# Kernel optimization log

Hardware: AMD Instinct MI355X
Metric: run time of the kernel (lower is better)

The kernel has to match this reference:

```python
import jax, jax.numpy as jnp
import numpy as np

D_MODEL = 768
NUM_HEADS = 12
DEPTH = D_MODEL // NUM_HEADS
LN_EPS = 1e-5


def setup_inputs() -> dict:
    key = jax.random.key(0)
    ks = jax.random.split(key, 5)
    B, S = 2, 2048
    scale = 1.0 / np.sqrt(D_MODEL)
    return {
        "Q": jax.random.normal(ks[0], (B, S, D_MODEL), jnp.float32),
        "W_q": jax.random.normal(ks[1], (D_MODEL, D_MODEL), jnp.float32) * scale,
        "b_q": jnp.zeros((D_MODEL,), jnp.float32),
        "W_k": jax.random.normal(ks[2], (D_MODEL, D_MODEL), jnp.float32) * scale,
        "b_k": jnp.zeros((D_MODEL,), jnp.float32),
        "W_v": jax.random.normal(ks[3], (D_MODEL, D_MODEL), jnp.float32) * scale,
        "b_v": jnp.zeros((D_MODEL,), jnp.float32),
        "W_o": jax.random.normal(ks[4], (D_MODEL, D_MODEL), jnp.float32) * scale,
        "b_o": jnp.zeros((D_MODEL,), jnp.float32),
        "ln_gamma": jnp.ones((D_MODEL,), jnp.float32),
        "ln_beta": jnp.zeros((D_MODEL,), jnp.float32),
    }


def _split_heads(x, B):
    # [B, S, D] -> [B, H, S, depth]
    return x.reshape(B, -1, NUM_HEADS, DEPTH).transpose(0, 2, 1, 3)


def reference(Q, W_q, b_q, W_k, b_k, W_v, b_v, W_o, b_o, ln_gamma, ln_beta):
    B = Q.shape[0]
    residual = Q
    # torch Linear: x @ W.T + b
    q = _split_heads(Q @ W_q.T + b_q, B)  # [B,H,S,dh]
    k = _split_heads(Q @ W_k.T + b_k, B)
    v = _split_heads(Q @ W_v.T + b_v, B)
    scores = jnp.einsum("bhqd,bhkd->bhqk", q, k) / jnp.sqrt(jnp.float32(DEPTH))
    attn = jax.nn.softmax(scores, axis=-1)
    out = jnp.einsum("bhqk,bhkd->bhqd", attn, v)
    out = out.transpose(0, 2, 1, 3).reshape(B, -1, D_MODEL)
    out = out @ W_o.T + b_o
    x = out + residual
    mu = jnp.mean(x, axis=-1, keepdims=True)
    var = jnp.mean(jnp.square(x - mu), axis=-1, keepdims=True)
    return (x - mu) * jax.lax.rsqrt(var + LN_EPS) * ln_gamma + ln_beta
```

## Files before the change

### kernel.cpp

```cpp
#include <hip/hip_runtime.h>
#include <hip/hip_bf16.h>

#define D_MODEL 768
#define S_LEN   2048
#define BATCH   2
#define NHEAD   12
#define DH      64
#define NTOK    (BATCH * S_LEN)
#define NBH     (BATCH * NHEAD)

typedef __attribute__((ext_vector_type(8))) short bf16x8;
typedef __attribute__((ext_vector_type(4))) float f32x4;

__device__ inline unsigned short f2bf(float f) {
    union { float f; unsigned u; } v; v.f = f;
    unsigned u = v.u;
    u += 0x7fffu + ((u >> 16) & 1u);
    return (unsigned short)(u >> 16);
}

__device__ inline unsigned pack_bf2(float a, float b) {
    union { __hip_bfloat162 h2; unsigned u; } cv;
    cv.h2 = __float22bfloat162_rn(make_float2(a, b));
    return cv.u;
}

__device__ inline float bf2f(unsigned short u) {
    union { unsigned u; float f; } c; c.u = ((unsigned)u) << 16; return c.f;
}

__device__ inline void stage16(const void* g, void* l) {
    __builtin_amdgcn_global_load_lds(
        (const __attribute__((address_space(1))) unsigned*)g,
        (__attribute__((address_space(3))) unsigned*)l, 16, 0, 0);
}

__global__ __launch_bounds__(256) void convert_kernel(
    const float* __restrict__ Q,
    const float* __restrict__ Wq, const float* __restrict__ Wk,
    const float* __restrict__ Wv, const float* __restrict__ Wo,
    unsigned short* __restrict__ Xb,
    unsigned short* __restrict__ Wqb, unsigned short* __restrict__ Wkb,
    unsigned short* __restrict__ Wvb, unsigned short* __restrict__ Wob)
{
    const int XV = NTOK * D_MODEL / 4;
    const int WV = D_MODEL * D_MODEL / 4;
    int idx = blockIdx.x * 256 + threadIdx.x;
    if (idx >= XV + 4 * WV) return;

    const float* src; unsigned short* dst; int off;
    if (idx < XV) { src = Q; dst = Xb; off = idx; }
    else {
        int i2 = idx - XV;
        int seg = i2 / WV; off = i2 - seg * WV;
        if      (seg == 0) { src = Wq; dst = Wqb; }
        else if (seg == 1) { src = Wk; dst = Wkb; }
        else if (seg == 2) { src = Wv; dst = Wvb; }
        else               { src = Wo; dst = Wob; }
    }
    float4 v = reinterpret_cast<const float4*>(src)[off];
    uint2 o;
    o.x = pack_bf2(v.x, v.y);
    o.y = pack_bf2(v.z, v.w);
    reinterpret_cast<uint2*>(dst)[off] = o;
}

#define STAGE_TILE(glob, rowstrideB, row0, k0, ldsbase, nIss)                 \
    _Pragma("unroll")                                                          \
    for (int i = 0; i < (nIss); ++i) {                                         \
        int L = i * 4096 + wv * 1024 + lane * 16;                              \
        int row = L >> 7;                                                      \
        int colb = (L & 127) ^ ((row & 7) << 4);                               \
        stage16((const char*)(glob) + (size_t)((row0) + row) * (rowstrideB)    \
                    + ((k0) << 1) + colb,                                      \
                (char*)(ldsbase) + i * 4096 + wv * 1024);                      \
    }

__global__ __launch_bounds__(256) void qkv_gemm_kernel(
    const unsigned short* __restrict__ Xb,
    const unsigned short* __restrict__ Wall,
    const float* __restrict__ bq, const float* __restrict__ bk,
    const float* __restrict__ bv,
    unsigned short* __restrict__ qb, unsigned short* __restrict__ kb,
    unsigned short* __restrict__ vtb)
{
    const int lane = threadIdx.x & 63;
    const int wv   = threadIdx.x >> 6;
    const int lr   = lane & 15;
    const int lg   = lane >> 4;
    const int wr   = wv >> 1;
    const int wc   = wv & 1;
    const int row0g = blockIdx.y * 128;
    const int col0g = blockIdx.x * 128;

    __shared__ __align__(16) unsigned short At[2][128 * 64];
    __shared__ __align__(16) unsigned short Bt[2][128 * 64];

    f32x4 acc[4][4] = {};

    STAGE_TILE(Xb,   1536, row0g, 0, At[0], 4);
    STAGE_TILE(Wall, 1536, col0g, 0, Bt[0], 4);
    __syncthreads();

    for (int s = 0; s < 12; ++s) {
        int cur = s & 1;
        if (s < 11) {
            STAGE_TILE(Xb,   1536, row0g, (s + 1) * 64, At[cur ^ 1], 4);
            STAGE_TILE(Wall, 1536, col0g, (s + 1) * 64, Bt[cur ^ 1], 4);
        }
        bf16x8 a[4][2], b[4][2];
#pragma unroll
        for (int mm = 0; mm < 4; ++mm) {
            int row = wr * 64 + mm * 16 + lr, sw = (row & 7) << 4;
#pragma unroll
            for (int ks = 0; ks < 2; ++ks)
                a[mm][ks] = *reinterpret_cast<const bf16x8*>(
                    (const char*)At[cur] + row * 128 + ((ks * 64 + lg * 16) ^ sw));
        }
#pragma unroll
        for (int n = 0; n < 4; ++n) {
            int row = wc * 64 + n * 16 + lr, sw = (row & 7) << 4;
#pragma unroll
            for (int ks = 0; ks < 2; ++ks)
                b[n][ks] = *reinterpret_cast<const bf16x8*>(
                    (const char*)Bt[cur] + row * 128 + ((ks * 64 + lg * 16) ^ sw));
        }
#pragma unroll
        for (int ks = 0; ks < 2; ++ks)
#pragma unroll
            for (int mm = 0; mm < 4; ++mm)
#pragma unroll
                for (int n = 0; n < 4; ++n)
                    acc[mm][n] = __builtin_amdgcn_mfma_f32_16x16x32_bf16(
                        a[mm][ks], b[n][ks], acc[mm][n], 0, 0, 0);
        __syncthreads();
    }

    const int which   = blockIdx.x / 6;
    const int colbase = (blockIdx.x % 6) * 128;
    const float* bias = (which == 0) ? bq : (which == 1) ? bk : bv;
#pragma unroll
    for (int mm = 0; mm < 4; ++mm) {
#pragma unroll
        for (int n = 0; n < 4; ++n) {
            int col = colbase + wc * 64 + n * 16 + lr;
            float bval = bias[col];
            int h = col >> 6, d = col & 63;
            int rowg = row0g + wr * 64 + mm * 16 + lg * 4;
            int bb = rowg >> 11, s0 = rowg & 2047;
            if (which == 2) {
                uint2 w;
                w.x = pack_bf2(acc[mm][n][0] + bval, acc[mm][n][1] + bval);
                w.y = pack_bf2(acc[mm][n][2] + bval, acc[mm][n][3] + bval);
                *reinterpret_cast<uint2*>(
                    vtb + ((size_t)(bb * NHEAD + h) * DH + d) * S_LEN + s0) = w;
            } else {
                unsigned short* dst = (which == 0) ? qb : kb;
#pragma unroll
                for (int r = 0; r < 4; ++r)
                    dst[((size_t)(bb * NHEAD + h) * S_LEN + s0 + r) * DH + d] =
                        f2bf(acc[mm][n][r] + bval);
            }
        }
    }
}

#define AC(BUF, DOSTAGE, VM)                                                   \
    {                                                                          \
        if (DOSTAGE) {                                                         \
            stage16(kg, sdK[((BUF) + 2) % 3]); kg += 8192;                     \
            stage16(vg, sdV[((BUF) + 2) % 3]); vg += 128;                      \
        }                                                                      \
        f32x4 s[4] = {};                                                       \
        __builtin_amdgcn_s_setprio(1);                                         \
        _Pragma("unroll")                                                      \
        for (int kt = 0; kt < 4; ++kt) {                                       \
            bf16x8 ak0 = *(const bf16x8*)(rdK[BUF] + kt * 2048);               \
            bf16x8 ak1 = *(const bf16x8*)(rdK[BUF] + kt * 2048 + oD);          \
            s[kt] = __builtin_amdgcn_mfma_f32_16x16x32_bf16(ak0, bq0, s[kt], 0, 0, 0); \
            s[kt] = __builtin_amdgcn_mfma_f32_16x16x32_bf16(ak1, bq1, s[kt], 0, 0, 0); \
        }                                                                      \
        __builtin_amdgcn_s_setprio(0);                                         \
        bf16x8 av0[4], av1[4];                                                 \
        _Pragma("unroll")                                                      \
        for (int t = 0; t < 4; ++t) {                                          \
            av0[t] = *(const bf16x8*)(rdV[BUF] + t * 2048);                    \
            av1[t] = *(const bf16x8*)(rdV[BUF] + t * 2048 + oD);               \
        }                                                                      \
        float g0 = fmaxf(fmaxf(s[0][0], s[0][1]), s[0][2]);                    \
        float g1 = fmaxf(fmaxf(s[0][3], s[1][0]), s[1][1]);                    \
        float g2 = fmaxf(fmaxf(s[1][2], s[1][3]), s[2][0]);                    \
        float g3 = fmaxf(fmaxf(s[2][1], s[2][2]), s[2][3]);                    \
        float g4 = fmaxf(fmaxf(s[3][0], s[3][1]), s[3][2]);                    \
        float mx = fmaxf(fmaxf(fmaxf(g0, g1), g2), fmaxf(fmaxf(g3, g4), s[3][3])); \
        if (__any(mx * SC > m + 8.0f)) {                                       \
            float mg = mx * SC;                                                \
            mg = fmaxf(mg, __shfl_xor(mg, 16));                                \
            mg = fmaxf(mg, __shfl_xor(mg, 32));                                \
            float mn = fmaxf(m, mg);                                           \
            float sf = __builtin_amdgcn_exp2f(m - mn);                         \
            m = mn; l *= sf;                                                   \
            _Pragma("unroll")                                                  \
            for (int t = 0; t < 4; ++t) acc[t] *= sf;                          \
        }                                                                      \
        float p[16];                                                           \
        _Pragma("unroll")                                                      \
        for (int kt = 0; kt < 4; ++kt)                                         \
            _Pragma("unroll")                                                  \
            for (int r = 0; r < 4; ++r)                                        \
                p[kt * 4 + r] = __builtin_amdgcn_exp2f(fmaf(s[kt][r], SC, -m)); \
        float sum = ((p[0] + p[1]) + (p[2] + p[3])) + ((p[4] + p[5]) + (p[6] + p[7])); \
        sum += ((p[8] + p[9]) + (p[10] + p[11])) + ((p[12] + p[13]) + (p[14] + p[15])); \
        l += sum;                                                              \
        _Pragma("unroll")                                                      \
        for (int kt = 0; kt < 4; ++kt) {                                       \
            uint2 w;                                                           \
            w.x = pack_bf2(p[kt * 4 + 0], p[kt * 4 + 1]);                      \
            w.y = pack_bf2(p[kt * 4 + 2], p[kt * 4 + 3]);                      \
            *(uint2*)(plw + kt * 32 + lg * 8) = w;                             \
        }                                                                      \
        union { bf16x8 v; uint2 u[2]; } bp0, bp1;                              \
        bp0.u[0] = *(const uint2*)(plr);                                       \
        bp0.u[1] = *(const uint2*)(plr + 8);                                   \
        bp1.u[0] = *(const uint2*)(plr + 64);                                  \
        bp1.u[1] = *(const uint2*)(plr + 72);                                  \
        __builtin_amdgcn_s_setprio(1);                                         \
        _Pragma("unroll")                                                      \
        for (int t = 0; t < 4; ++t) {                                          \
            acc[t] = __builtin_amdgcn_mfma_f32_16x16x32_bf16(av0[t], bp0.v, acc[t], 0, 0, 0); \
            acc[t] = __builtin_amdgcn_mfma_f32_16x16x32_bf16(av1[t], bp1.v, acc[t], 0, 0, 0); \
        }                                                                      \
        __builtin_amdgcn_s_setprio(0);                                         \
        if ((VM) == 2) {                                                       \
            asm volatile("s_waitcnt vmcnt(2)" ::: "memory");                   \
            __builtin_amdgcn_s_barrier();                                      \
        } else if ((VM) == 0) {                                                \
            asm volatile("s_waitcnt vmcnt(0)" ::: "memory");                   \
            __builtin_amdgcn_s_barrier();                                      \
        }                                                                      \
    }

template<int KS>
__global__ __launch_bounds__(512) void attn_kernel(
    const unsigned short* __restrict__ qb, const unsigned short* __restrict__ kb,
    const unsigned short* __restrict__ vtb,
    unsigned short* __restrict__ attnb,
    unsigned short* __restrict__ Opart,
    float2* __restrict__ mlbuf)
{
    const int lane = threadIdx.x & 63;
    const int wv   = threadIdx.x >> 6;
    const int lr   = lane & 15;
    const int lg   = lane >> 4;
    const int bh   = blockIdx.y;
    const int h    = bh % NHEAD, bb = bh / NHEAD;
    const int q0   = blockIdx.x * 128 + wv * 16;
    const int ks   = (KS == 2) ? blockIdx.z : 0;

    __shared__ __align__(16) unsigned short Kt[3][4096];
    __shared__ __align__(16) unsigned short Vt[3][4096];
    __shared__ __align__(16) unsigned short PL[8][16][68];

    const char* kbase = (const char*)(kb  + (size_t)bh * S_LEN * DH)
                        + (size_t)ks * (S_LEN / KS) * 128;
    const char* vbase = (const char*)(vtb + (size_t)bh * DH * S_LEN)
                        + (size_t)ks * (S_LEN / KS) * 2;
    const unsigned short* qptr = qb + ((size_t)bh * S_LEN + q0) * DH;

    bf16x8 bq0 = *reinterpret_cast<const bf16x8*>(qptr + (size_t)lr * DH + lg * 8);
    bf16x8 bq1 = *reinterpret_cast<const bf16x8*>(qptr + (size_t)lr * DH + 32 + lg * 8);

    const int swr = (lr & 7) << 4;
    const int o0  = (lg * 16) ^ swr;
    const int oD  = (o0 ^ 64) - o0;
    const int L1  = wv * 1024 + lane * 16;
    const int r1  = L1 >> 7;
    const int cb1 = (L1 & 127) ^ ((r1 & 7) << 4);

    const char* kg = kbase + (size_t)r1 * 128 + cb1;
    const char* vg = vbase + (size_t)r1 * 4096 + cb1;
    char* sdK[3] = { (char*)Kt[0] + wv * 1024, (char*)Kt[1] + wv * 1024,
                     (char*)Kt[2] + wv * 1024 };
    char* sdV[3] = { (char*)Vt[0] + wv * 1024, (char*)Vt[1] + wv * 1024,
                     (char*)Vt[2] + wv * 1024 };
    const char* rdK[3] = {
        (const char*)Kt[0] + lr * 128 + o0,
        (const char*)Kt[1] + lr * 128 + o0,
        (const char*)Kt[2] + lr * 128 + o0 };
    const char* rdV[3] = {
        (const char*)Vt[0] + lr * 128 + o0,
        (const char*)Vt[1] + lr * 128 + o0,
        (const char*)Vt[2] + lr * 128 + o0 };
    char* plw = (char*)PL + wv * 2176 + lr * 136;
    const char* plr = plw + lg * 16;

    float m = -1e30f, l = 0.f;
    f32x4 acc[4] = {};
    const float SC = 0.125f * 1.44269504088896f;

    stage16(kg, sdK[0]); kg += 8192;
    stage16(vg, sdV[0]); vg += 128;
    stage16(kg, sdK[1]); kg += 8192;
    stage16(vg, sdV[1]); vg += 128;
    asm volatile("s_waitcnt vmcnt(2)" ::: "memory");
    __builtin_amdgcn_s_barrier();

    if constexpr (KS == 2) {
        for (int it = 0; it < 4; ++it) {
            AC(0, 1, 2); AC(1, 1, 2); AC(2, 1, 2);
        }
        AC(0, 1, 2);
        AC(1, 1, 2);
        AC(2, 0, 0);
        AC(0, 0, -1);
    } else {
        for (int it = 0; it < 10; ++it) {
            AC(0, 1, 2); AC(1, 1, 2); AC(2, 1, 2);
        }
        AC(0, 0, 0);
        AC(1, 0, -1);
    }

    l += __shfl_xor(l, 16);
    l += __shfl_xor(l, 32);

    if constexpr (KS == 1) {
        float rl = 1.0f / l;
        size_t rowbase = ((size_t)(bb * S_LEN + q0 + lr)) * D_MODEL + h * DH;
#pragma unroll
        for (int t = 0; t < 4; ++t) {
            unsigned w0 = pack_bf2(acc[t][0] * rl, acc[t][1] * rl);
            unsigned w1 = pack_bf2(acc[t][2] * rl, acc[t][3] * rl);
            *reinterpret_cast<unsigned*>(attnb + rowbase + t * 16 + lg * 4)     = w0;
            *reinterpret_cast<unsigned*>(attnb + rowbase + t * 16 + lg * 4 + 2) = w1;
        }
    } else {
        size_t base = ((size_t)(ks * NBH + bh) * S_LEN + q0 + lr) * 64;
#pragma unroll
        for (int t = 0; t < 4; ++t) {
            unsigned w0 = pack_bf2(acc[t][0], acc[t][1]);
            unsigned w1 = pack_bf2(acc[t][2], acc[t][3]);
            *reinterpret_cast<unsigned*>(Opart + base + t * 16 + lg * 4)     = w0;
            *reinterpret_cast<unsigned*>(Opart + base + t * 16 + lg * 4 + 2) = w1;
        }
        if (lg == 0)
            mlbuf[(size_t)(ks * NBH + bh) * S_LEN + q0 + lr] = make_float2(m, l);
    }
}

__global__ __launch_bounds__(256) void combine_kernel(
    const unsigned short* __restrict__ Opart,
    const float2* __restrict__ mlbuf,
    unsigned short* __restrict__ attnb)
{
    int idx = blockIdx.x * 256 + threadIdx.x;
    int d4  = idx & 15;
    int h   = (idx >> 4) % 12;
    int tok = idx / 192;
    int bb  = tok >> 11, s = tok & 2047;
    size_t qoff = (size_t)(bb * NHEAD + h) * S_LEN + s;

    float2 ml0 = mlbuf[qoff];
    float2 ml1 = mlbuf[(size_t)NBH * S_LEN + qoff];
    float M  = fmaxf(ml0.x, ml1.x);
    float w0 = __builtin_amdgcn_exp2f(ml0.x - M);
    float w1 = __builtin_amdgcn_exp2f(ml1.x - M);
    float ri = 1.0f / (w0 * ml0.y + w1 * ml1.y);
    w0 *= ri; w1 *= ri;

    size_t ob = qoff * 64 + d4 * 4;
    ushort4 a = *reinterpret_cast<const ushort4*>(Opart + ob);
    ushort4 b = *reinterpret_cast<const ushort4*>(Opart + (size_t)NBH * S_LEN * 64 + ob);
    float o0 = bf2f(a.x) * w0 + bf2f(b.x) * w1;
    float o1 = bf2f(a.y) * w0 + bf2f(b.y) * w1;
    float o2 = bf2f(a.z) * w0 + bf2f(b.z) * w1;
    float o3 = bf2f(a.w) * w0 + bf2f(b.w) * w1;
    uint2 w;
    w.x = pack_bf2(o0, o1);
    w.y = pack_bf2(o2, o3);
    *reinterpret_cast<uint2*>(attnb + (size_t)tok * D_MODEL + h * 64 + d4 * 4) = w;
}

__global__ __launch_bounds__(256) void oproj_kernel(
    const unsigned short* __restrict__ attnb, const unsigned short* __restrict__ Wob,
    const float* __restrict__ bo, const float* __restrict__ Qres,
    float* __restrict__ Y)
{
    const int lane = threadIdx.x & 63;
    const int wv   = threadIdx.x >> 6;
    const int lr   = lane & 15;
    const int lg   = lane >> 4;
    const int row0g = blockIdx.y * 128;
    const int col0g = blockIdx.x * 64;

    __shared__ __align__(16) unsigned short At[2][128 * 64];
    __shared__ __align__(16) unsigned short Bt[2][64 * 64];

    f32x4 acc[2][4] = {};

    STAGE_TILE(attnb, 1536, row0g, 0, At[0], 4);
    STAGE_TILE(Wob,   1536, col0g, 0, Bt[0], 2);
    __syncthreads();

    for (int s = 0; s < 12; ++s) {
        int cur = s & 1;
        if (s < 11) {
            STAGE_TILE(attnb, 1536, row0g, (s + 1) * 64, At[cur ^ 1], 4);
            STAGE_TILE(Wob,   1536, col0g, (s + 1) * 64, Bt[cur ^ 1], 2);
        }
        bf16x8 a[2][2], b[4][2];
#pragma unroll
        for (int mm = 0; mm < 2; ++mm) {
            int row = wv * 32 + mm * 16 + lr, sw = (row & 7) << 4;
#pragma unroll
            for (int ks = 0; ks < 2; ++ks)
                a[mm][ks] = *reinterpret_cast<const bf16x8*>(
                    (const char*)At[cur] + row * 128 + ((ks * 64 + lg * 16) ^ sw));
        }
#pragma unroll
        for (int n = 0; n < 4; ++n) {
            int row = n * 16 + lr, sw = (row & 7) << 4;
#pragma unroll
            for (int ks = 0; ks < 2; ++ks)
                b[n][ks] = *reinterpret_cast<const bf16x8*>(
                    (const char*)Bt[cur] + row * 128 + ((ks * 64 + lg * 16) ^ sw));
        }
#pragma unroll
        for (int ks = 0; ks < 2; ++ks)
#pragma unroll
            for (int mm = 0; mm < 2; ++mm)
#pragma unroll
                for (int n = 0; n < 4; ++n)
                    acc[mm][n] = __builtin_amdgcn_mfma_f32_16x16x32_bf16(
                        a[mm][ks], b[n][ks], acc[mm][n], 0, 0, 0);
        __syncthreads();
    }

#pragma unroll
    for (int mm = 0; mm < 2; ++mm)
#pragma unroll
        for (int n = 0; n < 4; ++n) {
            int col = col0g + n * 16 + lr;
            float bval = bo[col];
#pragma unroll
            for (int r = 0; r < 4; ++r) {
                int row = row0g + wv * 32 + mm * 16 + lg * 4 + r;
                size_t off = (size_t)row * D_MODEL + col;
                Y[off] = acc[mm][n][r] + bval + Qres[off];
            }
        }
}

__global__ __launch_bounds__(256) void ln_kernel(
    const float* __restrict__ Y,
    const float* __restrict__ gamma, const float* __restrict__ beta,
    float* __restrict__ out)
{
    const int lane = threadIdx.x & 63;
    const int row  = blockIdx.x * 4 + (threadIdx.x >> 6);
    const float4* yr = reinterpret_cast<const float4*>(Y + (size_t)row * D_MODEL);

    float4 v[3];
    float sum = 0.f, ss = 0.f;
#pragma unroll
    for (int j = 0; j < 3; ++j) {
        v[j] = yr[lane + 64 * j];
        sum += v[j].x + v[j].y + v[j].z + v[j].w;
        ss  += v[j].x * v[j].x + v[j].y * v[j].y + v[j].z * v[j].z + v[j].w * v[j].w;
    }
#pragma unroll
    for (int msk = 1; msk < 64; msk <<= 1) {
        sum += __shfl_xor(sum, msk);
        ss  += __shfl_xor(ss,  msk);
    }
    float mu  = sum * (1.f / 768.f);
    float var = ss * (1.f / 768.f) - mu * mu;
    float is  = rsqrtf(var + 1e-5f);

    const float4* g4 = reinterpret_cast<const float4*>(gamma);
    const float4* b4 = reinterpret_cast<const float4*>(beta);
    float4* o4 = reinterpret_cast<float4*>(out + (size_t)row * D_MODEL);
#pragma unroll
    for (int j = 0; j < 3; ++j) {
        float4 g = g4[lane + 64 * j], b = b4[lane + 64 * j], r;
        r.x = (v[j].x - mu) * is * g.x + b.x;
        r.y = (v[j].y - mu) * is * g.y + b.y;
        r.z = (v[j].z - mu) * is * g.z + b.z;
        r.w = (v[j].w - mu) * is * g.w + b.w;
        o4[lane + 64 * j] = r;
    }
}

extern "C" void kernel_launch(void* const* d_in, const int* in_sizes, int n_in,
                              void* d_out, int out_size, void* d_ws, size_t ws_size,
                              hipStream_t stream)
{
    const float* Q     = (const float*)d_in[0];
    const float* Wq    = (const float*)d_in[1];
    const float* bq    = (const float*)d_in[2];
    const float* Wk    = (const float*)d_in[3];
    const float* bk    = (const float*)d_in[4];
    const float* Wv    = (const float*)d_in[5];
    const float* bv    = (const float*)d_in[6];
    const float* Wo    = (const float*)d_in[7];
    const float* bo    = (const float*)d_in[8];
    const float* gamma = (const float*)d_in[9];
    const float* beta  = (const float*)d_in[10];
    float* out = (float*)d_out;

    char* ws = (char*)d_ws;
    unsigned short* Xb    = (unsigned short*)(ws + 0);
    unsigned short* Wqb   = (unsigned short*)(ws + 6291456);
    unsigned short* Wkb   = (unsigned short*)(ws + 7471104);
    unsigned short* Wvb   = (unsigned short*)(ws + 8650752);
    unsigned short* Wob   = (unsigned short*)(ws + 9830400);
    unsigned short* qb    = (unsigned short*)(ws + 11010048);
    unsigned short* kb    = (unsigned short*)(ws + 17301504);
    unsigned short* vtb   = (unsigned short*)(ws + 23592960);
    unsigned short* attnb = (unsigned short*)(ws + 29884416);
    float*          Yf    = (float*)        (ws + 36175872);
    unsigned short* Opartb = (unsigned short*)(ws + 36175872);
    float2*         mlbuf  = (float2*)       (ws + 61341696);

    const bool splitk = (ws_size >= 62128128ull);

    convert_kernel<<<5376, 256, 0, stream>>>(Q, Wq, Wk, Wv, Wo, Xb, Wqb, Wkb, Wvb, Wob);
    qkv_gemm_kernel<<<dim3(18, 32), 256, 0, stream>>>(Xb, Wqb, bq, bk, bv, qb, kb, vtb);
    if (splitk) {
        attn_kernel<2><<<dim3(16, 24, 2), 512, 0, stream>>>(qb, kb, vtb, attnb,
                                                            Opartb, mlbuf);
        combine_kernel<<<3072, 256, 0, stream>>>(Opartb, mlbuf, attnb);
    } else {
        attn_kernel<1><<<dim3(16, 24), 512, 0, stream>>>(qb, kb, vtb, attnb,
                                                         Opartb, mlbuf);
    }
    oproj_kernel<<<dim3(12, 32), 256, 0, stream>>>(attnb, Wob, bo, Q, Yf);
    ln_kernel<<<1024, 256, 0, stream>>>(Yf, gamma, beta, out);
}
```

Baseline: 112.4 us.

## Process two 16-row query tiles per wave to reuse staged K/V tiles

Each wave now handles 32 query rows as two independent 16-row sub-tiles (A and B), each with its own running max, sum and accumulators, sharing every K fragment loaded from LDS. The per-block query span doubles to 256, so the attention grid halves in x. This halves the K/V LDS staging and global traffic per query row and amortizes the barriers. In exchange it roughly doubles accumulator and softmax register pressure, moves the V fragment loads inside the PV loop, and launches fewer blocks (192 or 384), which may leave CUs underused. Both sub-tiles write their probabilities through the same per-wave LDS scratch, so the second SMPV pass overwrites the first.

```diff
diff --git a/kernel.cpp b/kernel.cpp
--- a/kernel.cpp
+++ b/kernel.cpp
@@ -165,53 +165,33 @@
     }
 }
 
-#define AC(BUF, DOSTAGE, VM)                                                   \
+#define SMPV(BUF, S, M, L, ACC, BPTR)                                          \
     {                                                                          \
-        if (DOSTAGE) {                                                         \
-            stage16(kg, sdK[((BUF) + 2) % 3]); kg += 8192;                     \
-            stage16(vg, sdV[((BUF) + 2) % 3]); vg += 128;                      \
-        }                                                                      \
-        f32x4 s[4] = {};                                                       \
-        __builtin_amdgcn_s_setprio(1);                                         \
-        _Pragma("unroll")                                                      \
-        for (int kt = 0; kt < 4; ++kt) {                                       \
-            bf16x8 ak0 = *(const bf16x8*)(rdK[BUF] + kt * 2048);               \
-            bf16x8 ak1 = *(const bf16x8*)(rdK[BUF] + kt * 2048 + oD);          \
-            s[kt] = __builtin_amdgcn_mfma_f32_16x16x32_bf16(ak0, bq0, s[kt], 0, 0, 0); \
-            s[kt] = __builtin_amdgcn_mfma_f32_16x16x32_bf16(ak1, bq1, s[kt], 0, 0, 0); \
-        }                                                                      \
-        __builtin_amdgcn_s_setprio(0);                                         \
-        bf16x8 av0[4], av1[4];                                                 \
-        _Pragma("unroll")                                                      \
-        for (int t = 0; t < 4; ++t) {                                          \
-            av0[t] = *(const bf16x8*)(rdV[BUF] + t * 2048);                    \
-            av1[t] = *(const bf16x8*)(rdV[BUF] + t * 2048 + oD);               \
-        }                                                                      \
-        float g0 = fmaxf(fmaxf(s[0][0], s[0][1]), s[0][2]);                    \
-        float g1 = fmaxf(fmaxf(s[0][3], s[1][0]), s[1][1]);                    \
-        float g2 = fmaxf(fmaxf(s[1][2], s[1][3]), s[2][0]);                    \
-        float g3 = fmaxf(fmaxf(s[2][1], s[2][2]), s[2][3]);                    \
-        float g4 = fmaxf(fmaxf(s[3][0], s[3][1]), s[3][2]);                    \
-        float mx = fmaxf(fmaxf(fmaxf(g0, g1), g2), fmaxf(fmaxf(g3, g4), s[3][3])); \
-        if (__any(mx * SC > m + 8.0f)) {                                       \
+        float g0 = fmaxf(fmaxf(S[0][0], S[0][1]), S[0][2]);                    \
+        float g1 = fmaxf(fmaxf(S[0][3], S[1][0]), S[1][1]);                    \
+        float g2 = fmaxf(fmaxf(S[1][2], S[1][3]), S[2][0]);                    \
+        float g3 = fmaxf(fmaxf(S[2][1], S[2][2]), S[2][3]);                    \
+        float g4 = fmaxf(fmaxf(S[3][0], S[3][1]), S[3][2]);                    \
+        float mx = fmaxf(fmaxf(fmaxf(g0, g1), g2), fmaxf(fmaxf(g3, g4), S[3][3])); \
+        if (__any(mx * SC > M + 8.0f)) {                                       \
             float mg = mx * SC;                                                \
             mg = fmaxf(mg, __shfl_xor(mg, 16));                                \
             mg = fmaxf(mg, __shfl_xor(mg, 32));                                \
-            float mn = fmaxf(m, mg);                                           \
-            float sf = __builtin_amdgcn_exp2f(m - mn);                         \
-            m = mn; l *= sf;                                                   \
+            float mn = fmaxf(M, mg);                                           \
+            float sf = __builtin_amdgcn_exp2f(M - mn);                         \
+            M = mn; L *= sf;                                                   \
             _Pragma("unroll")                                                  \
-            for (int t = 0; t < 4; ++t) acc[t] *= sf;                          \
+            for (int t = 0; t < 4; ++t) ACC[t] *= sf;                          \
         }                                                                      \
         float p[16];                                                           \
         _Pragma("unroll")                                                      \
         for (int kt = 0; kt < 4; ++kt)                                         \
             _Pragma("unroll")                                                  \
             for (int r = 0; r < 4; ++r)                                        \
-                p[kt * 4 + r] = __builtin_amdgcn_exp2f(fmaf(s[kt][r], SC, -m)); \
+                p[kt * 4 + r] = __builtin_amdgcn_exp2f(fmaf(S[kt][r], SC, -M)); \
         float sum = ((p[0] + p[1]) + (p[2] + p[3])) + ((p[4] + p[5]) + (p[6] + p[7])); \
         sum += ((p[8] + p[9]) + (p[10] + p[11])) + ((p[12] + p[13]) + (p[14] + p[15])); \
-        l += sum;                                                              \
+        L += sum;                                                              \
         _Pragma("unroll")                                                      \
         for (int kt = 0; kt < 4; ++kt) {                                       \
             uint2 w;                                                           \
@@ -227,10 +207,34 @@
         __builtin_amdgcn_s_setprio(1);                                         \
         _Pragma("unroll")                                                      \
         for (int t = 0; t < 4; ++t) {                                          \
-            acc[t] = __builtin_amdgcn_mfma_f32_16x16x32_bf16(av0[t], bp0.v, acc[t], 0, 0, 0); \
-            acc[t] = __builtin_amdgcn_mfma_f32_16x16x32_bf16(av1[t], bp1.v, acc[t], 0, 0, 0); \
+            bf16x8 av0 = *(const bf16x8*)(rdV[BUF] + t * 2048);                \
+            bf16x8 av1 = *(const bf16x8*)(rdV[BUF] + t * 2048 + oD);           \
+            ACC[t] = __builtin_amdgcn_mfma_f32_16x16x32_bf16(av0, bp0.v, ACC[t], 0, 0, 0); \
+            ACC[t] = __builtin_amdgcn_mfma_f32_16x16x32_bf16(av1, bp1.v, ACC[t], 0, 0, 0); \
         }                                                                      \
         __builtin_amdgcn_s_setprio(0);                                         \
+    }
+
+#define AC(BUF, DOSTAGE, VM)                                                   \
+    {                                                                          \
+        if (DOSTAGE) {                                                         \
+            stage16(kg, sdK[((BUF) + 2) % 3]); kg += 8192;                     \
+            stage16(vg, sdV[((BUF) + 2) % 3]); vg += 128;                      \
+        }                                                                      \
+        f32x4 sA[4] = {}, sB[4] = {};                                          \
+        __builtin_amdgcn_s_setprio(1);                                         \
+        _Pragma("unroll")                                                      \
+        for (int kt = 0; kt < 4; ++kt) {                                       \
+            bf16x8 ak0 = *(const bf16x8*)(rdK[BUF] + kt * 2048);               \
+            bf16x8 ak1 = *(const bf16x8*)(rdK[BUF] + kt * 2048 + oD);          \
+            sA[kt] = __builtin_amdgcn_mfma_f32_16x16x32_bf16(ak0, bqA0, sA[kt], 0, 0, 0); \
+            sB[kt] = __builtin_amdgcn_mfma_f32_16x16x32_bf16(ak0, bqB0, sB[kt], 0, 0, 0); \
+            sA[kt] = __builtin_amdgcn_mfma_f32_16x16x32_bf16(ak1, bqA1, sA[kt], 0, 0, 0); \
+            sB[kt] = __builtin_amdgcn_mfma_f32_16x16x32_bf16(ak1, bqB1, sB[kt], 0, 0, 0); \
+        }                                                                      \
+        __builtin_amdgcn_s_setprio(0);                                         \
+        SMPV(BUF, sA, mA, lA, accA, plr)                                       \
+        SMPV(BUF, sB, mB, lB, accB, plr)                                       \
         if ((VM) == 2) {                                                       \
             asm volatile("s_waitcnt vmcnt(2)" ::: "memory");                   \
             __builtin_amdgcn_s_barrier();                                      \
@@ -254,7 +258,7 @@
     const int lg   = lane >> 4;
     const int bh   = blockIdx.y;
     const int h    = bh % NHEAD, bb = bh / NHEAD;
-    const int q0   = blockIdx.x * 128 + wv * 16;
+    const int q0   = blockIdx.x * 256 + wv * 32;
     const int ks   = (KS == 2) ? blockIdx.z : 0;
 
     __shared__ __align__(16) unsigned short Kt[3][4096];
@@ -267,8 +271,10 @@
                         + (size_t)ks * (S_LEN / KS) * 2;
     const unsigned short* qptr = qb + ((size_t)bh * S_LEN + q0) * DH;
 
-    bf16x8 bq0 = *reinterpret_cast<const bf16x8*>(qptr + (size_t)lr * DH + lg * 8);
-    bf16x8 bq1 = *reinterpret_cast<const bf16x8*>(qptr + (size_t)lr * DH + 32 + lg * 8);
+    bf16x8 bqA0 = *reinterpret_cast<const bf16x8*>(qptr + (size_t)lr * DH + lg * 8);
+    bf16x8 bqA1 = *reinterpret_cast<const bf16x8*>(qptr + (size_t)lr * DH + 32 + lg * 8);
+    bf16x8 bqB0 = *reinterpret_cast<const bf16x8*>(qptr + (size_t)(16 + lr) * DH + lg * 8);
+    bf16x8 bqB1 = *reinterpret_cast<const bf16x8*>(qptr + (size_t)(16 + lr) * DH + 32 + lg * 8);
 
     const int swr = (lr & 7) << 4;
     const int o0  = (lg * 16) ^ swr;
@@ -294,8 +300,8 @@
     char* plw = (char*)PL + wv * 2176 + lr * 136;
     const char* plr = plw + lg * 16;
 
-    float m = -1e30f, l = 0.f;
-    f32x4 acc[4] = {};
+    float mA = -1e30f, lA = 0.f, mB = -1e30f, lB = 0.f;
+    f32x4 accA[4] = {}, accB[4] = {};
     const float SC = 0.125f * 1.44269504088896f;
 
     stage16(kg, sdK[0]); kg += 8192;
@@ -321,30 +327,42 @@
         AC(1, 0, -1);
     }
 
-    l += __shfl_xor(l, 16);
-    l += __shfl_xor(l, 32);
+    lA += __shfl_xor(lA, 16); lA += __shfl_xor(lA, 32);
+    lB += __shfl_xor(lB, 16); lB += __shfl_xor(lB, 32);
 
     if constexpr (KS == 1) {
-        float rl = 1.0f / l;
-        size_t rowbase = ((size_t)(bb * S_LEN + q0 + lr)) * D_MODEL + h * DH;
+        float rlA = 1.0f / lA, rlB = 1.0f / lB;
+        size_t rbA = ((size_t)(bb * S_LEN + q0 + lr)) * D_MODEL + h * DH;
+        size_t rbB = ((size_t)(bb * S_LEN + q0 + 16 + lr)) * D_MODEL + h * DH;
 #pragma unroll
         for (int t = 0; t < 4; ++t) {
-            unsigned w0 = pack_bf2(acc[t][0] * rl, acc[t][1] * rl);
-            unsigned w1 = pack_bf2(acc[t][2] * rl, acc[t][3] * rl);
-            *reinterpret_cast<unsigned*>(attnb + rowbase + t * 16 + lg * 4)     = w0;
-            *reinterpret_cast<unsigned*>(attnb + rowbase + t * 16 + lg * 4 + 2) = w1;
+            *reinterpret_cast<unsigned*>(attnb + rbA + t * 16 + lg * 4) =
+                pack_bf2(accA[t][0] * rlA, accA[t][1] * rlA);
+            *reinterpret_cast<unsigned*>(attnb + rbA + t * 16 + lg * 4 + 2) =
+                pack_bf2(accA[t][2] * rlA, accA[t][3] * rlA);
+            *reinterpret_cast<unsigned*>(attnb + rbB + t * 16 + lg * 4) =
+                pack_bf2(accB[t][0] * rlB, accB[t][1] * rlB);
+            *reinterpret_cast<unsigned*>(attnb + rbB + t * 16 + lg * 4 + 2) =
+                pack_bf2(accB[t][2] * rlB, accB[t][3] * rlB);
         }
     } else {
-        size_t base = ((size_t)(ks * NBH + bh) * S_LEN + q0 + lr) * 64;
+        size_t baseA = ((size_t)(ks * NBH + bh) * S_LEN + q0 + lr) * 64;
+        size_t baseB = ((size_t)(ks * NBH + bh) * S_LEN + q0 + 16 + lr) * 64;
 #pragma unroll
         for (int t = 0; t < 4; ++t) {
-            unsigned w0 = pack_bf2(acc[t][0], acc[t][1]);
-            unsigned w1 = pack_bf2(acc[t][2], acc[t][3]);
-            *reinterpret_cast<unsigned*>(Opart + base + t * 16 + lg * 4)     = w0;
-            *reinterpret_cast<unsigned*>(Opart + base + t * 16 + lg * 4 + 2) = w1;
-        }
-        if (lg == 0)
-            mlbuf[(size_t)(ks * NBH + bh) * S_LEN + q0 + lr] = make_float2(m, l);
+            *reinterpret_cast<unsigned*>(Opart + baseA + t * 16 + lg * 4) =
+                pack_bf2(accA[t][0], accA[t][1]);
+            *reinterpret_cast<unsigned*>(Opart + baseA + t * 16 + lg * 4 + 2) =
+                pack_bf2(accA[t][2], accA[t][3]);
+            *reinterpret_cast<unsigned*>(Opart + baseB + t * 16 + lg * 4) =
+                pack_bf2(accB[t][0], accB[t][1]);
+            *reinterpret_cast<unsigned*>(Opart + baseB + t * 16 + lg * 4 + 2) =
+                pack_bf2(accB[t][2], accB[t][3]);
+        }
+        if (lg == 0) {
+            mlbuf[(size_t)(ks * NBH + bh) * S_LEN + q0 + lr]      = make_float2(mA, lA);
+            mlbuf[(size_t)(ks * NBH + bh) * S_LEN + q0 + 16 + lr] = make_float2(mB, lB);
+        }
     }
 }
 
@@ -527,12 +545,12 @@
     convert_kernel<<<5376, 256, 0, stream>>>(Q, Wq, Wk, Wv, Wo, Xb, Wqb, Wkb, Wvb, Wob);
     qkv_gemm_kernel<<<dim3(18, 32), 256, 0, stream>>>(Xb, Wqb, bq, bk, bv, qb, kb, vtb);
     if (splitk) {
-        attn_kernel<2><<<dim3(16, 24, 2), 512, 0, stream>>>(qb, kb, vtb, attnb,
-                                                            Opartb, mlbuf);
+        attn_kernel<2><<<dim3(8, 24, 2), 512, 0, stream>>>(qb, kb, vtb, attnb,
+                                                           Opartb, mlbuf);
         combine_kernel<<<3072, 256, 0, stream>>>(Opartb, mlbuf, attnb);
     } else {
-        attn_kernel<1><<<dim3(16, 24), 512, 0, stream>>>(qb, kb, vtb, attnb,
-                                                         Opartb, mlbuf);
+        attn_kernel<1><<<dim3(8, 24), 512, 0, stream>>>(qb, kb, vtb, attnb,
+                                                        Opartb, mlbuf);
     }
     oproj_kernel<<<dim3(12, 32), 256, 0, stream>>>(attnb, Wob, bo, Q, Yf);
     ln_kernel<<<1024, 256, 0, stream>>>(Yf, gamma, beta, out);
```

Measured after the change: 128.6 us. 14.4% more time.
